# Optimization experiments

Hardware: AMD Instinct MI355X
Metric: run time of the kernel (lower is better)

## Reference

```python
import jax, jax.numpy as jnp
import numpy as np

EPS = 1e-6
N_REP = 4  # num_heads // num_kv_heads


def _qk_norm(a):
    a32 = a.astype(jnp.float32)
    var = jnp.mean(jnp.square(a32), axis=-1, keepdims=True)
    return (a32 * jax.lax.rsqrt(var + EPS)).astype(a.dtype)


def setup_inputs() -> dict:
    key = jax.random.key(0)
    ks = jax.random.split(key, 5)
    B, Tq, C, H, D, Hkv = 2, 2048, 2048, 16, 128, 4
    s = 0.02
    return {
        "x_q": jax.random.normal(ks[0], (B, Tq, C), dtype=jnp.float32),
        "Wq": jax.random.normal(ks[1], (C, H, D), dtype=jnp.float32) * s,
        "Wk": jax.random.normal(ks[2], (C, Hkv, D), dtype=jnp.float32) * s,
        "Wv": jax.random.normal(ks[3], (C, Hkv, D), dtype=jnp.float32) * s,
        "Wo": jax.random.normal(ks[4], (H * D, C), dtype=jnp.float32) * s,
    }


def reference(x_q, Wq, Wk, Wv, Wo):
    # x_q: (B, Tq, C); self-attention (x_kv = x_q)
    B, Tq, C = x_q.shape
    D = Wq.shape[-1]
    q = jnp.einsum('btc,chd->bthd', x_q, Wq)   # (B,Tq,H,D)
    k = jnp.einsum('btc,chd->bthd', x_q, Wk)   # (B,Tq,Hkv,D)
    v = jnp.einsum('btc,chd->bthd', x_q, Wv)
    # per-head QK RMS-norm
    q = _qk_norm(q)
    k = _qk_norm(k)
    # GQA: repeat kv heads (each kv head repeated N_REP times consecutively)
    k = jnp.repeat(k, N_REP, axis=2)           # (B,Tq,H,D)
    v = jnp.repeat(v, N_REP, axis=2)
    scale = jnp.asarray(1.0 / np.sqrt(D), dtype=q.dtype)
    logits = jnp.einsum('bqhd,bkhd->bhqk', q, k) * scale
    attn = jax.nn.softmax(logits, axis=-1)
    out = jnp.einsum('bhqk,bkhd->bqhd', attn, v)
    out = out.reshape(B, Tq, -1)               # (B,Tq,H*D)
    return out @ Wo                            # (B,Tq,C)
```

## Files before the change

### kernel.cpp

```cpp
#include <hip/hip_runtime.h>

typedef __attribute__((ext_vector_type(4))) float f32x4;
typedef __attribute__((ext_vector_type(16))) float f32x16;
typedef __attribute__((ext_vector_type(8))) short bf16x8;
typedef __attribute__((ext_vector_type(4))) unsigned u32x4;

#define DEV __device__ __forceinline__

DEV unsigned short f2bf(float f) {
  unsigned u = __float_as_uint(f);
  unsigned r = (u + 0x7FFFu + ((u >> 16) & 1u)) >> 16;
  return (unsigned short)r;
}
DEV float bf2f(unsigned short h) { return __uint_as_float(((unsigned)h) << 16); }

DEV unsigned cvtpk(float lo, float hi) {
  unsigned r;
  asm("v_cvt_pk_bf16_f32 %0, %1, %2" : "=v"(r) : "v"(lo), "v"(hi));
  return r;
}
DEV bf16x8 frag4(unsigned a, unsigned b, unsigned c, unsigned d) {
  u32x4 u = {a, b, c, d};
  return __builtin_bit_cast(bf16x8, u);
}

typedef __attribute__((address_space(1))) void gas_t;
typedef __attribute__((address_space(3))) void las_t;
DEV void async16(void* lds, const void* g) {
  __builtin_amdgcn_global_load_lds((gas_t*)g, (las_t*)lds, 16, 0, 0);
}

__global__ void cast_x(const float* __restrict__ x, unsigned short* __restrict__ y, int n8) {
  int idx = blockIdx.x * blockDim.x + threadIdx.x;
  int stride = gridDim.x * blockDim.x;
  for (; idx < n8; idx += stride) {
    const float4* p = (const float4*)(x + (size_t)idx * 8);
    float4 v0 = p[0], v1 = p[1];
    bf16x8 o;
    o[0] = (short)f2bf(v0.x); o[1] = (short)f2bf(v0.y);
    o[2] = (short)f2bf(v0.z); o[3] = (short)f2bf(v0.w);
    o[4] = (short)f2bf(v1.x); o[5] = (short)f2bf(v1.y);
    o[6] = (short)f2bf(v1.z); o[7] = (short)f2bf(v1.w);
    *(bf16x8*)(y + (size_t)idx * 8) = o;
  }
}

__global__ void transpose_cast(const float* __restrict__ W, unsigned short* __restrict__ Wt,
                               int Kdim, int Nw) {
  __shared__ float tile[32][33];
  int n0 = blockIdx.x * 32, k0 = blockIdx.y * 32;
  int tx = threadIdx.x, ty = threadIdx.y;
#pragma unroll
  for (int r = ty; r < 32; r += 8)
    tile[r][tx] = W[(size_t)(k0 + r) * Nw + n0 + tx];
  __syncthreads();
#pragma unroll
  for (int r = ty; r < 32; r += 8)
    Wt[(size_t)(n0 + r) * Kdim + k0 + tx] = f2bf(tile[tx][r]);
}

template <int EPI>
__global__ __launch_bounds__(256, 2)
void gemm_bt(const unsigned short* __restrict__ A, const unsigned short* __restrict__ Bt,
             int Kr, float* __restrict__ Cf, int Nr,
             unsigned short* __restrict__ Qn, unsigned short* __restrict__ Kn,
             unsigned short* __restrict__ Vt) {
  __shared__ __align__(16) unsigned short lsA[128 * 32];
  __shared__ __align__(16) unsigned short lsB[128 * 32];
  const int t = threadIdx.x;
  const int lane = t & 63;
  const int w = t >> 6, wr = w >> 1, wc = w & 1;
  const int lo = lane & 15, hi = lane >> 4;
  const int nwg = gridDim.x * 32;
  const int bid0 = blockIdx.y * gridDim.x + blockIdx.x;
  const int sw = (bid0 & 7) * (nwg >> 3) + (bid0 >> 3);
  const int m0 = (sw & 31) * 128, n0 = (sw >> 5) * 128;

  const int c0 = t, c1 = t + 256;
  const unsigned short* gA0 = A + (size_t)(m0 + (c0 >> 2)) * Kr + (c0 & 3) * 8;
  const unsigned short* gA1 = A + (size_t)(m0 + (c1 >> 2)) * Kr + (c1 & 3) * 8;
  const unsigned short* gB0 = Bt + (size_t)(n0 + (c0 >> 2)) * Kr + (c0 & 3) * 8;
  const unsigned short* gB1 = Bt + (size_t)(n0 + (c1 >> 2)) * Kr + (c1 & 3) * 8;
  unsigned short* lA0 = lsA + c0 * 8;
  unsigned short* lA1 = lsA + c1 * 8;
  unsigned short* lB0 = lsB + c0 * 8;
  unsigned short* lB1 = lsB + c1 * 8;

  f32x4 acc[4][4] = {};

  for (int kt = 0; kt < Kr; kt += 32) {
    async16(lA0, gA0 + kt);
    async16(lA1, gA1 + kt);
    async16(lB0, gB0 + kt);
    async16(lB1, gB1 + kt);
    __syncthreads();
    bf16x8 af[4], bfr[4];
#pragma unroll
    for (int i = 0; i < 4; ++i) {
      af[i]  = *(const bf16x8*)&lsA[(wr * 64 + i * 16 + lo) * 32 + hi * 8];
      bfr[i] = *(const bf16x8*)&lsB[(wc * 64 + i * 16 + lo) * 32 + hi * 8];
    }
#pragma unroll
    for (int mi = 0; mi < 4; ++mi)
#pragma unroll
      for (int ni = 0; ni < 4; ++ni)
        acc[mi][ni] = __builtin_amdgcn_mfma_f32_16x16x32_bf16(af[mi], bfr[ni], acc[mi][ni], 0, 0, 0);
    __syncthreads();
  }

#pragma unroll
  for (int mi = 0; mi < 4; ++mi)
#pragma unroll
    for (int ni = 0; ni < 4; ++ni)
#pragma unroll
      for (int i = 0; i < 4; ++i) {
        int gm = m0 + wr * 64 + mi * 16 + hi * 4 + i;
        int gn = n0 + wc * 64 + ni * 16 + lo;
        float v = acc[mi][ni][i];
        if (EPI == 0) {
          Cf[(size_t)gm * Nr + gn] = v;
        } else {
          unsigned short bv = f2bf(v);
          int bb = gm >> 11, tt = gm & 2047;
          if (gn < 2048) {
            int hh = gn >> 7, dd = gn & 127;
            Qn[(((size_t)bb * 16 + hh) * 2048 + tt) * 128 + dd] = bv;
          } else if (gn < 2560) {
            int g2 = gn - 2048, hh = g2 >> 7, dd = g2 & 127;
            Kn[(((size_t)bb * 4 + hh) * 2048 + tt) * 128 + dd] = bv;
          } else {
            int g2 = gn - 2560, hh = g2 >> 7, dd = g2 & 127;
            Vt[(((size_t)bb * 4 + hh) * 128 + dd) * 2048 + tt] = bv;
          }
        }
      }
}

__global__ __launch_bounds__(256)
void qk_norm(unsigned short* __restrict__ Qn, unsigned short* __restrict__ Kn, float qscale) {
  int row = blockIdx.x * 4 + (threadIdx.x >> 6);
  int lane = threadIdx.x & 63;
  unsigned short* base;
  float scl;
  if (row < 65536) { base = Qn + (size_t)row * 128; scl = qscale; }
  else             { base = Kn + (size_t)(row - 65536) * 128; scl = 1.0f; }
  unsigned v = *(const unsigned*)(base + lane * 2);
  float a = bf2f((unsigned short)(v & 0xffffu));
  float b = bf2f((unsigned short)(v >> 16));
  float ss = a * a + b * b;
#pragma unroll
  for (int m = 1; m < 64; m <<= 1) ss += __shfl_xor(ss, m, 64);
  float r = rsqrtf(ss * (1.0f / 128.0f) + 1e-6f) * scl;
  *(unsigned*)(base + lane * 2) = ((unsigned)f2bf(b * r) << 16) | (unsigned)f2bf(a * r);
}

__global__ __launch_bounds__(256)
void fragV(const unsigned short* __restrict__ Vt, unsigned short* __restrict__ Vf) {
  int tid = blockIdx.x * 256 + threadIdx.x;
  int bhkv = tid >> 15, c = tid & 32767;
  int lane = c & 63, tile = c >> 10, mid = (c >> 6) & 15;
  int dt = mid >> 2, g2 = mid & 3;
  int d = dt * 32 + (lane & 31);
  int g = g2 * 2 + (lane >> 5);
  int k0 = tile * 64 + g * 8;
  const uint4* src = (const uint4*)(Vt + ((size_t)bhkv * 128 + d) * 2048 + k0);
  uint4* dst = (uint4*)(Vf + (size_t)bhkv * 262144 + (size_t)c * 8);
  *dst = *src;
}

__global__ __launch_bounds__(256, 2)
void attn(const unsigned short* __restrict__ Q, const unsigned short* __restrict__ Kk,
          const unsigned short* __restrict__ Vf, unsigned short* __restrict__ AO) {
  const int bid = blockIdx.x;
  const int x = bid & 7, r2 = bid >> 3;
  const int h2 = r2 & 3, qx = r2 >> 2;
  const int b = x >> 2, hkv = x & 3;
  const int h = hkv * 4 + h2, bh = b * 16 + h, bhkv = b * 4 + hkv;
  const int t = threadIdx.x;
  const int w = t >> 6, lane = t & 63;
  const int qi = lane & 31, h1 = lane >> 5;
  const unsigned short* Qb = Q  + (size_t)bh * 2048 * 128;
  const unsigned short* Kb = Kk + (size_t)bhkv * 2048 * 128;
  const unsigned short* Vfb = Vf + (size_t)bhkv * 262144;
  const int q0 = qx * 128 + w * 32;

  __shared__ __align__(16) unsigned short Klds[2][64 * 128];

  bf16x8 qf[8];
#pragma unroll
  for (int s = 0; s < 8; ++s)
    qf[s] = *(const bf16x8*)&Qb[(size_t)(q0 + qi) * 128 + s * 16 + h1 * 8];

  f32x16 Oc[4] = {};
  float mrow = -1e30f, srow = 0.f;

#define STAGE_K(bufi, kt_)                                                       \
  {                                                                              \
    const unsigned short* gK = Kb + (size_t)(kt_) * 128;                         \
    _Pragma("unroll")                                                            \
    for (int j = 0; j < 4; ++j) {                                                \
      int gi = j * 256 + t;                                                      \
      int kr = gi >> 4, kg = (gi & 15) ^ (kr & 15);                              \
      async16(&Klds[bufi][gi * 8], gK + (size_t)kr * 128 + kg * 8);              \
    }                                                                            \
  }

  STAGE_K(0, 0);
  __syncthreads();

  int cur = 0;
  for (int ti = 0; ti < 32; ++ti) {
    if (ti + 1 < 32) STAGE_K(cur ^ 1, (ti + 1) * 64);

    bf16x8 vf0[2][4], vf1[2][4];
#pragma unroll
    for (int mt = 0; mt < 2; ++mt)
#pragma unroll
      for (int dt = 0; dt < 4; ++dt) {
        const unsigned short* vp = Vfb + ((size_t)((ti * 4 + dt) * 4 + mt * 2)) * 512 + lane * 8;
        vf0[mt][dt] = *(const bf16x8*)(vp);
        vf1[mt][dt] = *(const bf16x8*)(vp + 512);
      }

    const unsigned short* KL = Klds[cur];

    f32x16 S[2] = {};
    __builtin_amdgcn_s_setprio(1);
#pragma unroll
    for (int mt = 0; mt < 2; ++mt) {
      const int krow = mt * 32 + qi;
      const unsigned short* krp = KL + krow * 128;
      const int rswz = krow & 15;
#pragma unroll
      for (int s = 0; s < 8; ++s) {
        bf16x8 kf = *(const bf16x8*)(krp + (((2 * s + h1) ^ rswz) << 3));
        S[mt] = __builtin_amdgcn_mfma_f32_32x32x16_bf16(kf, qf[s], S[mt], 0, 0, 0);
      }
    }
    __builtin_amdgcn_s_setprio(0);

    float t8[8];
#pragma unroll
    for (int r = 0; r < 8; ++r)
      t8[r] = fmaxf(fmaxf(S[0][r], S[0][r + 8]), fmaxf(S[1][r], S[1][r + 8]));
#pragma unroll
    for (int r = 0; r < 4; ++r) t8[r] = fmaxf(t8[r], t8[r + 4]);
    float mx = fmaxf(fmaxf(t8[0], t8[1]), fmaxf(t8[2], t8[3]));
    mx = fmaxf(mx, __shfl_xor(mx, 32, 64));
    if (__any(mx > mrow + 8.0f)) {
      float mnew = fmaxf(mrow, mx);
      float al = __builtin_amdgcn_exp2f(mrow - mnew);
      mrow = mnew;
      srow *= al;
#pragma unroll
      for (int dt = 0; dt < 4; ++dt)
#pragma unroll
        for (int r = 0; r < 16; ++r) Oc[dt][r] *= al;
    }
#pragma unroll
    for (int mt = 0; mt < 2; ++mt)
#pragma unroll
      for (int r = 0; r < 16; ++r)
        S[mt][r] = __builtin_amdgcn_exp2f(S[mt][r] - mrow);
    float s8[8];
#pragma unroll
    for (int r = 0; r < 8; ++r)
      s8[r] = (S[0][r] + S[0][r + 8]) + (S[1][r] + S[1][r + 8]);
#pragma unroll
    for (int r = 0; r < 4; ++r) s8[r] += s8[r + 4];
    float rs = (s8[0] + s8[1]) + (s8[2] + s8[3]);
    rs += __shfl_xor(rs, 32, 64);
    srow += rs;

    __builtin_amdgcn_s_setprio(1);
#pragma unroll
    for (int mt = 0; mt < 2; ++mt) {
      unsigned wd[8];
#pragma unroll
      for (int i2 = 0; i2 < 8; ++i2) wd[i2] = cvtpk(S[mt][2 * i2], S[mt][2 * i2 + 1]);
      unsigned r0 = __shfl_xor(h1 ? wd[0] : wd[2], 32, 64);
      unsigned r1 = __shfl_xor(h1 ? wd[1] : wd[3], 32, 64);
      unsigned r2_ = __shfl_xor(h1 ? wd[4] : wd[6], 32, 64);
      unsigned r3 = __shfl_xor(h1 ? wd[5] : wd[7], 32, 64);
      bf16x8 pf0 = frag4(h1 ? r0 : wd[0], h1 ? r1 : wd[1], h1 ? wd[2] : r0, h1 ? wd[3] : r1);
      bf16x8 pf1 = frag4(h1 ? r2_ : wd[4], h1 ? r3 : wd[5], h1 ? wd[6] : r2_, h1 ? wd[7] : r3);
#pragma unroll
      for (int dt = 0; dt < 4; ++dt) {
        Oc[dt] = __builtin_amdgcn_mfma_f32_32x32x16_bf16(vf0[mt][dt], pf0, Oc[dt], 0, 0, 0);
        Oc[dt] = __builtin_amdgcn_mfma_f32_32x32x16_bf16(vf1[mt][dt], pf1, Oc[dt], 0, 0, 0);
      }
    }
    __builtin_amdgcn_s_setprio(0);

    __syncthreads();
    cur ^= 1;
  }

  const float inv = 1.0f / srow;
  const size_t orow = ((size_t)(b * 2048 + q0 + qi)) * 2048 + h * 128;
#pragma unroll
  for (int dt = 0; dt < 4; ++dt)
#pragma unroll
    for (int rq = 0; rq < 4; ++rq) {
      int d0 = dt * 32 + 8 * rq + 4 * h1;
      unsigned u0 = cvtpk(Oc[dt][4 * rq + 0] * inv, Oc[dt][4 * rq + 1] * inv);
      unsigned u1 = cvtpk(Oc[dt][4 * rq + 2] * inv, Oc[dt][4 * rq + 3] * inv);
      uint2 st = {u0, u1};
      *(uint2*)((unsigned short*)AO + orow + d0) = st;
    }
}

extern "C" void kernel_launch(void* const* d_in, const int* in_sizes, int n_in,
                              void* d_out, int out_size, void* d_ws, size_t ws_size,
                              hipStream_t stream) {
  const float* x_q = (const float*)d_in[0];
  const float* Wq  = (const float*)d_in[1];
  const float* Wk  = (const float*)d_in[2];
  const float* Wv  = (const float*)d_in[3];
  const float* Wo  = (const float*)d_in[4];
  float* out = (float*)d_out;

  char* ws = (char*)d_ws;
  unsigned short* Xb    = (unsigned short*)(ws);
  unsigned short* WqkvT = (unsigned short*)(ws + 16777216);
  unsigned short* WoT   = (unsigned short*)(ws + 29360128);
  unsigned short* Qn    = (unsigned short*)(ws + 37748736);
  unsigned short* Kn    = (unsigned short*)(ws + 54525952);
  unsigned short* Vt    = (unsigned short*)(ws + 58720256);
  unsigned short* AO    = Xb;
  unsigned short* Vf    = WqkvT;

  cast_x<<<2048, 256, 0, stream>>>(x_q, Xb, (4096 * 2048) / 8);
  transpose_cast<<<dim3(2048 / 32, 2048 / 32), dim3(32, 8), 0, stream>>>(Wq, WqkvT, 2048, 2048);
  transpose_cast<<<dim3(512 / 32, 2048 / 32), dim3(32, 8), 0, stream>>>(Wk, WqkvT + 2048 * 2048, 2048, 512);
  transpose_cast<<<dim3(512 / 32, 2048 / 32), dim3(32, 8), 0, stream>>>(Wv, WqkvT + 2560 * 2048, 2048, 512);
  transpose_cast<<<dim3(2048 / 32, 2048 / 32), dim3(32, 8), 0, stream>>>(Wo, WoT, 2048, 2048);

  gemm_bt<1><<<dim3(3072 / 128, 4096 / 128), 256, 0, stream>>>(Xb, WqkvT, 2048, nullptr, 0, Qn, Kn, Vt);
  qk_norm<<<(65536 + 16384) / 4, 256, 0, stream>>>(Qn, Kn, 0.12751742f);
  fragV<<<1024, 256, 0, stream>>>(Vt, Vf);
  attn<<<512, 256, 0, stream>>>(Qn, Kn, Vf, AO);
  gemm_bt<0><<<dim3(2048 / 128, 4096 / 128), 256, 0, stream>>>(AO, WoT, 2048, out, 2048,
                                                               nullptr, nullptr, nullptr);
}
```

Before: 255.9 us.

## Rewrite bf16 GEMM as 256x128 triple-buffered swizzled LDS pipeline with 8 waves

```diff
diff --git a/kernel.cpp b/kernel.cpp
--- a/kernel.cpp
+++ b/kernel.cpp
@@ -60,52 +60,85 @@
 }
 
 template <int EPI>
-__global__ __launch_bounds__(256, 2)
+__global__ __launch_bounds__(512, 1)
 void gemm_bt(const unsigned short* __restrict__ A, const unsigned short* __restrict__ Bt,
              int Kr, float* __restrict__ Cf, int Nr,
              unsigned short* __restrict__ Qn, unsigned short* __restrict__ Kn,
              unsigned short* __restrict__ Vt) {
-  __shared__ __align__(16) unsigned short lsA[128 * 32];
-  __shared__ __align__(16) unsigned short lsB[128 * 32];
-  const int t = threadIdx.x;
-  const int lane = t & 63;
-  const int w = t >> 6, wr = w >> 1, wc = w & 1;
+  __shared__ __align__(16) unsigned short Lds[3 * 24576];
+  const int t = threadIdx.x, lane = t & 63;
+  const int w = t >> 6, wm = w >> 1, wn = w & 1;
   const int lo = lane & 15, hi = lane >> 4;
-  const int nwg = gridDim.x * 32;
-  const int bid0 = blockIdx.y * gridDim.x + blockIdx.x;
+  const int swz8 = lo & 7;
+  const int nwg = gridDim.x;
+  const int bid0 = blockIdx.x;
   const int sw = (bid0 & 7) * (nwg >> 3) + (bid0 >> 3);
-  const int m0 = (sw & 31) * 128, n0 = (sw >> 5) * 128;
-
-  const int c0 = t, c1 = t + 256;
-  const unsigned short* gA0 = A + (size_t)(m0 + (c0 >> 2)) * Kr + (c0 & 3) * 8;
-  const unsigned short* gA1 = A + (size_t)(m0 + (c1 >> 2)) * Kr + (c1 & 3) * 8;
-  const unsigned short* gB0 = Bt + (size_t)(n0 + (c0 >> 2)) * Kr + (c0 & 3) * 8;
-  const unsigned short* gB1 = Bt + (size_t)(n0 + (c1 >> 2)) * Kr + (c1 & 3) * 8;
-  unsigned short* lA0 = lsA + c0 * 8;
-  unsigned short* lA1 = lsA + c1 * 8;
-  unsigned short* lB0 = lsB + c0 * 8;
-  unsigned short* lB1 = lsB + c1 * 8;
+  const int m0 = (sw & 15) * 256, n0 = (sw >> 4) * 128;
+
+  unsigned short* b0 = Lds;
+  unsigned short* b1 = Lds + 24576;
+  unsigned short* b2 = Lds + 49152;
+
+#define SG_A(buf, kt_, u_) { int gi = (u_) * 512 + t; int rw = gi >> 3;              \
+    int g = (gi & 7) ^ (rw & 7);                                                     \
+    async16((buf) + gi * 8, A + (size_t)(m0 + rw) * Kr + (kt_) + g * 8); }
+#define SG_B(buf, kt_, u_) { int gi = (u_) * 512 + t; int rw = gi >> 3;              \
+    int g = (gi & 7) ^ (rw & 7);                                                     \
+    async16((buf) + 16384 + gi * 8, Bt + (size_t)(n0 + rw) * Kr + (kt_) + g * 8); }
 
   f32x4 acc[4][4] = {};
 
-  for (int kt = 0; kt < Kr; kt += 32) {
-    async16(lA0, gA0 + kt);
-    async16(lA1, gA1 + kt);
-    async16(lB0, gB0 + kt);
-    async16(lB1, gB1 + kt);
-    __syncthreads();
-    bf16x8 af[4], bfr[4];
-#pragma unroll
-    for (int i = 0; i < 4; ++i) {
-      af[i]  = *(const bf16x8*)&lsA[(wr * 64 + i * 16 + lo) * 32 + hi * 8];
-      bfr[i] = *(const bf16x8*)&lsB[(wc * 64 + i * 16 + lo) * 32 + hi * 8];
-    }
-#pragma unroll
-    for (int mi = 0; mi < 4; ++mi)
-#pragma unroll
-      for (int ni = 0; ni < 4; ++ni)
-        acc[mi][ni] = __builtin_amdgcn_mfma_f32_16x16x32_bf16(af[mi], bfr[ni], acc[mi][ni], 0, 0, 0);
-    __syncthreads();
+  SG_A(b0, 0, 0) SG_A(b0, 0, 1) SG_A(b0, 0, 2) SG_A(b0, 0, 3)
+  SG_B(b0, 0, 0) SG_B(b0, 0, 1)
+  SG_A(b1, 64, 0) SG_A(b1, 64, 1) SG_A(b1, 64, 2) SG_A(b1, 64, 3)
+  SG_B(b1, 64, 0) SG_B(b1, 64, 1)
+  asm volatile("s_waitcnt vmcnt(6)" ::: "memory");
+  __builtin_amdgcn_s_barrier();
+
+  const int nt = Kr >> 6;
+  for (int j = 0; j < nt; ++j) {
+    const bool pf = (j + 2 < nt);
+    const int kt2 = (j + 2) << 6;
+    bf16x8 bfr[4][2];
+#pragma unroll
+    for (int p = 0; p < 4; ++p) {
+      bf16x8 af[2];
+      {
+        const unsigned short* ab = b0 + (wm * 64 + p * 16 + lo) * 64;
+        af[0] = *(const bf16x8*)(ab + (((0 + hi) ^ swz8) << 3));
+        af[1] = *(const bf16x8*)(ab + (((4 + hi) ^ swz8) << 3));
+      }
+      if (p == 0) {
+#pragma unroll
+        for (int nn = 0; nn < 4; ++nn) {
+          const unsigned short* bb = b0 + 16384 + (wn * 64 + nn * 16 + lo) * 64;
+          bfr[nn][0] = *(const bf16x8*)(bb + (((0 + hi) ^ swz8) << 3));
+          bfr[nn][1] = *(const bf16x8*)(bb + (((4 + hi) ^ swz8) << 3));
+        }
+      }
+      if (pf) {
+        if (p == 0)      { SG_A(b2, kt2, 0) SG_A(b2, kt2, 1) }
+        else if (p == 1) { SG_A(b2, kt2, 2) SG_A(b2, kt2, 3) }
+        else if (p == 2) { SG_B(b2, kt2, 0) }
+        else             { SG_B(b2, kt2, 1) }
+      }
+      __builtin_amdgcn_s_barrier();
+      asm volatile("s_waitcnt lgkmcnt(0)" ::: "memory");
+      __builtin_amdgcn_sched_barrier(0);
+      __builtin_amdgcn_s_setprio(1);
+#pragma unroll
+      for (int nn = 0; nn < 4; ++nn) {
+        acc[p][nn] = __builtin_amdgcn_mfma_f32_16x16x32_bf16(af[0], bfr[nn][0], acc[p][nn], 0, 0, 0);
+        acc[p][nn] = __builtin_amdgcn_mfma_f32_16x16x32_bf16(af[1], bfr[nn][1], acc[p][nn], 0, 0, 0);
+      }
+      __builtin_amdgcn_s_setprio(0);
+      if (p == 3) {
+        if (pf) asm volatile("s_waitcnt vmcnt(6)" ::: "memory");
+        else    asm volatile("s_waitcnt vmcnt(0)" ::: "memory");
+      }
+      __builtin_amdgcn_s_barrier();
+    }
+    unsigned short* tb = b0; b0 = b1; b1 = b2; b2 = tb;
   }
 
 #pragma unroll
@@ -114,8 +147,8 @@
     for (int ni = 0; ni < 4; ++ni)
 #pragma unroll
       for (int i = 0; i < 4; ++i) {
-        int gm = m0 + wr * 64 + mi * 16 + hi * 4 + i;
-        int gn = n0 + wc * 64 + ni * 16 + lo;
+        int gm = m0 + wm * 64 + mi * 16 + hi * 4 + i;
+        int gn = n0 + wn * 64 + ni * 16 + lo;
         float v = acc[mi][ni][i];
         if (EPI == 0) {
           Cf[(size_t)gm * Nr + gn] = v;
@@ -336,10 +369,10 @@
   transpose_cast<<<dim3(512 / 32, 2048 / 32), dim3(32, 8), 0, stream>>>(Wv, WqkvT + 2560 * 2048, 2048, 512);
   transpose_cast<<<dim3(2048 / 32, 2048 / 32), dim3(32, 8), 0, stream>>>(Wo, WoT, 2048, 2048);
 
-  gemm_bt<1><<<dim3(3072 / 128, 4096 / 128), 256, 0, stream>>>(Xb, WqkvT, 2048, nullptr, 0, Qn, Kn, Vt);
+  gemm_bt<1><<<384, 512, 0, stream>>>(Xb, WqkvT, 2048, nullptr, 0, Qn, Kn, Vt);
   qk_norm<<<(65536 + 16384) / 4, 256, 0, stream>>>(Qn, Kn, 0.12751742f);
   fragV<<<1024, 256, 0, stream>>>(Vt, Vf);
   attn<<<512, 256, 0, stream>>>(Qn, Kn, Vf, AO);
-  gemm_bt<0><<<dim3(2048 / 128, 4096 / 128), 256, 0, stream>>>(AO, WoT, 2048, out, 2048,
-                                                               nullptr, nullptr, nullptr);
-}
+  gemm_bt<0><<<256, 512, 0, stream>>>(AO, WoT, 2048, out, 2048,
+                                      nullptr, nullptr, nullptr);
+}
```

Measured after the change: 261.7 us. +2.3%, slower.
